# Optimization experiments

Hardware: AMD Instinct MI355X
Metric: run time of the kernel (lower is better)

## Reference

```python
import jax, jax.numpy as jnp
import numpy as np
import math

EMB = 512

def setup_inputs() -> dict:
    key = jax.random.key(0)
    ks = jax.random.split(key, 7)
    B, L, E = 4, 4096, EMB
    s = 1.0 / math.sqrt(E)
    return {
        "x": jax.random.normal(ks[0], (B, L, E), dtype=jnp.float32),
        "Wq": jax.random.normal(ks[1], (E, E), dtype=jnp.float32) * s,
        "bq": jax.random.normal(ks[2], (E,), dtype=jnp.float32) * 0.01,
        "Wk": jax.random.normal(ks[3], (E, E), dtype=jnp.float32) * s,
        "bk": jax.random.normal(ks[4], (E,), dtype=jnp.float32) * 0.01,
        "Wv": jax.random.normal(ks[5], (E, E), dtype=jnp.float32) * s,
        "bv": jax.random.normal(ks[6], (E,), dtype=jnp.float32) * 0.01,
    }

def reference(x, Wq, bq, Wk, bk, Wv, bv):
    # x: [B, L, E]; Linear weights stored torch-style [out, in]
    E = x.shape[-1]
    L = x.shape[1]
    q = jnp.einsum('ble,fe->blf', x, Wq) + bq
    k = jnp.einsum('ble,fe->blf', x, Wk) + bk
    v = jnp.einsum('ble,fe->blf', x, Wv) + bv
    qk = jnp.einsum('bqe,bke->bqk', q, k)  # [B, L, L]
    # causal mask: strict upper triangle filled with -1e9 BEFORE scaling (as in source)
    mask = jnp.triu(jnp.ones((L, L), dtype=bool), k=1)
    qk = jnp.where(mask, jnp.float32(-1e9), qk)
    att = jax.nn.softmax(qk / jnp.sqrt(jnp.float32(E)), axis=-1)
    return jnp.einsum('bqk,bke->bqe', att, v)
```

## Files before the change

### kernel.cpp

```cpp
#include <hip/hip_runtime.h>

typedef unsigned short u16;
typedef short bf16x8 __attribute__((ext_vector_type(8)));
typedef float f32x4 __attribute__((ext_vector_type(4)));
typedef u16 u16x8 __attribute__((ext_vector_type(8)));
typedef u16 u16x4 __attribute__((ext_vector_type(4)));

#define LQ   4096
#define EMB  512
#define NB   4
#define MROWS (NB * LQ)
#define QSCALE 0.04419417382415922f

__device__ __forceinline__ u16 f2bf(float f) {
  unsigned u = __builtin_bit_cast(unsigned, f);
  u += 0x7fffu + ((u >> 16) & 1u);
  return (u16)(u >> 16);
}
__device__ __forceinline__ float bf2f(u16 h) {
  unsigned u = ((unsigned)h) << 16;
  return __builtin_bit_cast(float, u);
}

__global__ void prep_w(const float* __restrict__ Wq, const float* __restrict__ bq,
                       const float* __restrict__ Wk, const float* __restrict__ bk,
                       const float* __restrict__ Wv, const float* __restrict__ bv,
                       u16* __restrict__ wqb, u16* __restrict__ wkb, u16* __restrict__ wvb,
                       float* __restrict__ bias) {
  int i = blockIdx.x * 256 + threadIdx.x;
  if (i < EMB * EMB) {
    wqb[i] = f2bf(Wq[i] * QSCALE);
    wkb[i] = f2bf(Wk[i]);
    wvb[i] = f2bf(Wv[i]);
  }
  if (i < EMB) {
    bias[i]           = bq[i] * QSCALE;
    bias[EMB + i]     = bk[i];
    bias[2 * EMB + i] = bv[i];
  }
}

__global__ void prep_x(const float* __restrict__ x, u16* __restrict__ xb) {
  int i = blockIdx.x * 256 + threadIdx.x;
  const float4* p = (const float4*)(x + (size_t)i * 8);
  float4 a = p[0], b = p[1];
  u16x8 o;
  o[0] = f2bf(a.x); o[1] = f2bf(a.y); o[2] = f2bf(a.z); o[3] = f2bf(a.w);
  o[4] = f2bf(b.x); o[5] = f2bf(b.y); o[6] = f2bf(b.z); o[7] = f2bf(b.w);
  *(u16x8*)(xb + (size_t)i * 8) = o;
}

__device__ __forceinline__ void gemm_tile_core(
    const u16* __restrict__ A, int lda,
    const u16* __restrict__ B, int ldb,
    int kIters, u16* ldsA, u16* ldsB,
    f32x4 acc[4][4], int tid, int lane, int wr, int wc)
{
  for (int kb = 0; kb < kIters; ++kb) {
    const u16* ga = A + kb * 64;
    const u16* gb = B + kb * 64;
#pragma unroll
    for (int p = 0; p < 4; ++p) {
      int c = tid + p * 256;
      int row = c >> 3, h = c & 7;
      int hh = h ^ (row & 7);
      uint4 va = *(const uint4*)(ga + (size_t)row * lda + h * 8);
      uint4 vb = *(const uint4*)(gb + (size_t)row * ldb + h * 8);
      *(uint4*)(ldsA + row * 64 + hh * 8) = va;
      *(uint4*)(ldsB + row * 64 + hh * 8) = vb;
    }
    __syncthreads();
#pragma unroll
    for (int s = 0; s < 2; ++s) {
      bf16x8 af[4], bf[4];
#pragma unroll
      for (int m = 0; m < 4; ++m) {
        int row = wr * 64 + m * 16 + (lane & 15);
        int hh = (s * 4 + (lane >> 4)) ^ (row & 7);
        af[m] = *(const bf16x8*)(ldsA + row * 64 + hh * 8);
      }
#pragma unroll
      for (int n = 0; n < 4; ++n) {
        int row = wc * 64 + n * 16 + (lane & 15);
        int hh = (s * 4 + (lane >> 4)) ^ (row & 7);
        bf[n] = *(const bf16x8*)(ldsB + row * 64 + hh * 8);
      }
#pragma unroll
      for (int m = 0; m < 4; ++m)
#pragma unroll
        for (int n = 0; n < 4; ++n)
          acc[m][n] = __builtin_amdgcn_mfma_f32_16x16x32_bf16(af[m], bf[n], acc[m][n], 0, 0, 0);
    }
    __syncthreads();
  }
}

template <int VT>
__global__ __launch_bounds__(256, 2) void k_qkv(
    const u16* __restrict__ xb, const u16* __restrict__ W,
    const float* __restrict__ bias, u16* __restrict__ out)
{
  __shared__ uint4 ldsraw[2048];
  u16* ldsA = (u16*)ldsraw;
  u16* ldsB = (u16*)(ldsraw + 1024);
  int bi = blockIdx.x;
  int rt = bi >> 2, ct = bi & 3;
  int tid = threadIdx.x, lane = tid & 63, wave = tid >> 6;
  int wr = wave >> 1, wc = wave & 1;
  f32x4 acc[4][4];
#pragma unroll
  for (int m = 0; m < 4; ++m)
#pragma unroll
    for (int n = 0; n < 4; ++n) acc[m][n] = (f32x4)0.0f;

  gemm_tile_core(xb + (size_t)rt * 128 * EMB, EMB,
                 W + (size_t)ct * 128 * EMB, EMB, EMB / 64,
                 ldsA, ldsB, acc, tid, lane, wr, wc);

#pragma unroll
  for (int m = 0; m < 4; ++m)
#pragma unroll
    for (int n = 0; n < 4; ++n) {
      int row0 = rt * 128 + wr * 64 + m * 16 + ((lane >> 4) << 2);
      int col  = ct * 128 + wc * 64 + n * 16 + (lane & 15);
      float bv = bias[col];
      if (VT == 0) {
#pragma unroll
        for (int r = 0; r < 4; ++r)
          out[(size_t)(row0 + r) * EMB + col] = f2bf(acc[m][n][r] + bv);
      } else {
        int b = row0 >> 12, l0 = row0 & (LQ - 1);
        u16x4 pk;
#pragma unroll
        for (int r = 0; r < 4; ++r) pk[r] = f2bf(acc[m][n][r] + bv);
        *(u16x4*)(out + ((size_t)(b * EMB + col)) * LQ + l0) = pk;
      }
    }
}

__global__ __launch_bounds__(256, 2) void k_qk(
    const u16* __restrict__ Q, const u16* __restrict__ K,
    u16* __restrict__ S, int bstart)
{
  __shared__ uint4 ldsraw[2048];
  u16* ldsA = (u16*)ldsraw;
  u16* ldsB = (u16*)(ldsraw + 1024);
  int t = blockIdx.x;
  int b_local = t / 528;
  int i = t - b_local * 528;
  int qi = (int)((sqrtf(8.f * (float)i + 1.f) - 1.f) * 0.5f);
  while ((qi + 1) * (qi + 2) / 2 <= i) ++qi;
  while (qi * (qi + 1) / 2 > i) --qi;
  int ki = i - qi * (qi + 1) / 2;
  int bg = bstart + b_local;

  int tid = threadIdx.x, lane = tid & 63, wave = tid >> 6;
  int wr = wave >> 1, wc = wave & 1;
  f32x4 acc[4][4];
#pragma unroll
  for (int m = 0; m < 4; ++m)
#pragma unroll
    for (int n = 0; n < 4; ++n) acc[m][n] = (f32x4)0.0f;

  gemm_tile_core(Q + ((size_t)bg * LQ + qi * 128) * EMB, EMB,
                 K + ((size_t)bg * LQ + ki * 128) * EMB, EMB, EMB / 64,
                 ldsA, ldsB, acc, tid, lane, wr, wc);

  u16* Sb = S + (size_t)b_local * LQ * LQ;
#pragma unroll
  for (int m = 0; m < 4; ++m)
#pragma unroll
    for (int n = 0; n < 4; ++n) {
      int row0 = qi * 128 + wr * 64 + m * 16 + ((lane >> 4) << 2);
      int col  = ki * 128 + wc * 64 + n * 16 + (lane & 15);
#pragma unroll
      for (int r = 0; r < 4; ++r) {
        int row = row0 + r;
        float v = (col > row) ? -1e9f : acc[m][n][r];
        Sb[(size_t)row * LQ + col] = f2bf(v);
      }
    }
}

__global__ __launch_bounds__(256) void k_softmax(u16* __restrict__ S)
{
  int rowb = blockIdx.x;
  int q = rowb & (LQ - 1);
  u16* sr = S + (size_t)rowb * LQ;
  int n = ((q >> 7) + 1) << 7;
  int tid = threadIdx.x;
  int lane = tid & 63, wave = tid >> 6;
  __shared__ float red[8];

  float v[16];
  float mx = -3.0e38f;
#pragma unroll
  for (int p = 0; p < 2; ++p) {
    int idx = (p * 256 + tid) * 8;
    if (idx < n) {
      u16x8 raw = *(const u16x8*)(sr + idx);
#pragma unroll
      for (int j = 0; j < 8; ++j) {
        float f = bf2f(raw[j]);
        v[p * 8 + j] = f;
        mx = fmaxf(mx, f);
      }
    }
  }
#pragma unroll
  for (int off = 32; off >= 1; off >>= 1) mx = fmaxf(mx, __shfl_xor(mx, off));
  if (lane == 0) red[wave] = mx;
  __syncthreads();
  if (tid == 0) red[4] = fmaxf(fmaxf(red[0], red[1]), fmaxf(red[2], red[3]));
  __syncthreads();
  mx = red[4];
  __syncthreads();

  float sum = 0.f;
#pragma unroll
  for (int p = 0; p < 2; ++p) {
    int idx = (p * 256 + tid) * 8;
    if (idx < n) {
#pragma unroll
      for (int j = 0; j < 8; ++j) {
        float e = __expf(v[p * 8 + j] - mx);
        v[p * 8 + j] = e;
        sum += e;
      }
    }
  }
#pragma unroll
  for (int off = 32; off >= 1; off >>= 1) sum += __shfl_xor(sum, off);
  if (lane == 0) red[wave] = sum;
  __syncthreads();
  if (tid == 0) red[4] = red[0] + red[1] + red[2] + red[3];
  __syncthreads();
  float inv = 1.0f / red[4];

#pragma unroll
  for (int p = 0; p < 2; ++p) {
    int idx = (p * 256 + tid) * 8;
    if (idx < n) {
      u16x8 o;
#pragma unroll
      for (int j = 0; j < 8; ++j) o[j] = f2bf(v[p * 8 + j] * inv);
      *(u16x8*)(sr + idx) = o;
    }
  }
}

__global__ __launch_bounds__(256, 2) void k_pv(
    const u16* __restrict__ P, const u16* __restrict__ Vt,
    float* __restrict__ out, int bstart, int bcount)
{
  __shared__ uint4 ldsraw[2048];
  u16* ldsA = (u16*)ldsraw;
  u16* ldsB = (u16*)(ldsraw + 1024);
  int bi = blockIdx.x;
  int per_rt = bcount * 4;
  int rt = 31 - bi / per_rt;
  int rem = bi % per_rt;
  int b_local = rem >> 2, ct = rem & 3;
  int bg = bstart + b_local;

  int tid = threadIdx.x, lane = tid & 63, wave = tid >> 6;
  int wr = wave >> 1, wc = wave & 1;
  f32x4 acc[4][4];
#pragma unroll
  for (int m = 0; m < 4; ++m)
#pragma unroll
    for (int n = 0; n < 4; ++n) acc[m][n] = (f32x4)0.0f;

  int kIters = (rt + 1) * 2;
  gemm_tile_core(P + (size_t)b_local * LQ * LQ + (size_t)rt * 128 * LQ, LQ,
                 Vt + ((size_t)bg * EMB + ct * 128) * LQ, LQ, kIters,
                 ldsA, ldsB, acc, tid, lane, wr, wc);

#pragma unroll
  for (int m = 0; m < 4; ++m)
#pragma unroll
    for (int n = 0; n < 4; ++n) {
      int row0 = rt * 128 + wr * 64 + m * 16 + ((lane >> 4) << 2);
      int col  = ct * 128 + wc * 64 + n * 16 + (lane & 15);
#pragma unroll
      for (int r = 0; r < 4; ++r)
        out[((size_t)bg * LQ + row0 + r) * EMB + col] = acc[m][n][r];
    }
}

extern "C" void kernel_launch(void* const* d_in, const int* in_sizes, int n_in,
                              void* d_out, int out_size, void* d_ws, size_t ws_size,
                              hipStream_t stream) {
  const float* x  = (const float*)d_in[0];
  const float* Wq = (const float*)d_in[1];
  const float* bq = (const float*)d_in[2];
  const float* Wk = (const float*)d_in[3];
  const float* bk = (const float*)d_in[4];
  const float* Wv = (const float*)d_in[5];
  const float* bv = (const float*)d_in[6];

  char* ws = (char*)d_ws;
  size_t off = 0;
  u16* xb  = (u16*)(ws + off); off += (size_t)MROWS * EMB * 2;
  u16* wqb = (u16*)(ws + off); off += (size_t)EMB * EMB * 2;
  u16* wkb = (u16*)(ws + off); off += (size_t)EMB * EMB * 2;
  u16* wvb = (u16*)(ws + off); off += (size_t)EMB * EMB * 2;
  float* bias = (float*)(ws + off); off += 3 * EMB * 4;
  off = (off + 255) & ~(size_t)255;
  u16* Qb  = (u16*)(ws + off); off += (size_t)MROWS * EMB * 2;
  u16* Kb  = (u16*)(ws + off); off += (size_t)MROWS * EMB * 2;
  u16* Vtb = (u16*)(ws + off); off += (size_t)MROWS * EMB * 2;
  size_t fixed = off;
  size_t s_full = (size_t)NB * LQ * LQ * 2;
  int bcap = (ws_size >= fixed + s_full) ? NB : 1;
  u16* Sb = (u16*)(ws + fixed);

  prep_w<<<(EMB * EMB + 255) / 256, 256, 0, stream>>>(Wq, bq, Wk, bk, Wv, bv,
                                                      wqb, wkb, wvb, bias);
  prep_x<<<(MROWS * EMB / 8) / 256, 256, 0, stream>>>(x, xb);

  k_qkv<0><<<512, 256, 0, stream>>>(xb, wqb, bias, Qb);
  k_qkv<0><<<512, 256, 0, stream>>>(xb, wkb, bias + EMB, Kb);
  k_qkv<1><<<512, 256, 0, stream>>>(xb, wvb, bias + 2 * EMB, Vtb);

  for (int bs = 0; bs < NB; bs += bcap) {
    int bc = (bs + bcap <= NB) ? bcap : (NB - bs);
    k_qk<<<528 * bc, 256, 0, stream>>>(Qb, Kb, Sb, bs);
    k_softmax<<<bc * LQ, 256, 0, stream>>>(Sb);
    k_pv<<<32 * bc * 4, 256, 0, stream>>>(Sb, Vtb, (float*)d_out, bs, bc);
  }
}
```

Before: 219.0 us.

## Use direct global-to-LDS loads, merge QKV launches, reorder PV tiles

Global-to-shared staging in the GEMM core now uses global_load_lds, which writes straight into LDS and skips the register round trip. The XOR swizzle moves from the LDS address to the global source address so the stored layout stays the same. The three QKV projection launches become one 1536-block launch, cutting launch count and keeping more blocks in flight. PV row tiles are also reordered so the long causal tiles go first and the short ones fill in after.

```diff
diff --git a/kernel.cpp b/kernel.cpp
--- a/kernel.cpp
+++ b/kernel.cpp
@@ -1,10 +1,14 @@
 #include <hip/hip_runtime.h>
 
 typedef unsigned short u16;
+typedef unsigned int u32;
 typedef short bf16x8 __attribute__((ext_vector_type(8)));
 typedef float f32x4 __attribute__((ext_vector_type(4)));
 typedef u16 u16x8 __attribute__((ext_vector_type(8)));
 typedef u16 u16x4 __attribute__((ext_vector_type(4)));
+
+typedef const __attribute__((address_space(1))) u32* gas_ptr;
+typedef __attribute__((address_space(3))) u32* las_ptr;
 
 #define LQ   4096
 #define EMB  512
@@ -56,23 +60,26 @@
     int kIters, u16* ldsA, u16* ldsB,
     f32x4 acc[4][4], int tid, int lane, int wr, int wc)
 {
+  int wave = tid >> 6;
   for (int kb = 0; kb < kIters; ++kb) {
     const u16* ga = A + kb * 64;
     const u16* gb = B + kb * 64;
 #pragma unroll
     for (int p = 0; p < 4; ++p) {
       int c = tid + p * 256;
-      int row = c >> 3, h = c & 7;
-      int hh = h ^ (row & 7);
-      uint4 va = *(const uint4*)(ga + (size_t)row * lda + h * 8);
-      uint4 vb = *(const uint4*)(gb + (size_t)row * ldb + h * 8);
-      *(uint4*)(ldsA + row * 64 + hh * 8) = va;
-      *(uint4*)(ldsB + row * 64 + hh * 8) = vb;
+      int row = c >> 3, hh = c & 7;
+      int h = hh ^ (row & 7);
+      const u16* sa = ga + (size_t)row * lda + h * 8;
+      const u16* sb = gb + (size_t)row * ldb + h * 8;
+      u16* la = ldsA + wave * 512 + p * 2048;
+      u16* lb = ldsB + wave * 512 + p * 2048;
+      __builtin_amdgcn_global_load_lds((gas_ptr)(const void*)sa, (las_ptr)(void*)la, 16, 0, 0);
+      __builtin_amdgcn_global_load_lds((gas_ptr)(const void*)sb, (las_ptr)(void*)lb, 16, 0, 0);
     }
     __syncthreads();
 #pragma unroll
     for (int s = 0; s < 2; ++s) {
-      bf16x8 af[4], bf[4];
+      bf16x8 af[4], bfr[4];
 #pragma unroll
       for (int m = 0; m < 4; ++m) {
         int row = wr * 64 + m * 16 + (lane & 15);
@@ -83,28 +90,33 @@
       for (int n = 0; n < 4; ++n) {
         int row = wc * 64 + n * 16 + (lane & 15);
         int hh = (s * 4 + (lane >> 4)) ^ (row & 7);
-        bf[n] = *(const bf16x8*)(ldsB + row * 64 + hh * 8);
+        bfr[n] = *(const bf16x8*)(ldsB + row * 64 + hh * 8);
       }
 #pragma unroll
       for (int m = 0; m < 4; ++m)
 #pragma unroll
         for (int n = 0; n < 4; ++n)
-          acc[m][n] = __builtin_amdgcn_mfma_f32_16x16x32_bf16(af[m], bf[n], acc[m][n], 0, 0, 0);
+          acc[m][n] = __builtin_amdgcn_mfma_f32_16x16x32_bf16(af[m], bfr[n], acc[m][n], 0, 0, 0);
     }
     __syncthreads();
   }
 }
 
-template <int VT>
 __global__ __launch_bounds__(256, 2) void k_qkv(
-    const u16* __restrict__ xb, const u16* __restrict__ W,
-    const float* __restrict__ bias, u16* __restrict__ out)
+    const u16* __restrict__ xb,
+    const u16* __restrict__ w0, const u16* __restrict__ w1, const u16* __restrict__ w2,
+    const float* __restrict__ bias,
+    u16* __restrict__ o0, u16* __restrict__ o1, u16* __restrict__ o2)
 {
   __shared__ uint4 ldsraw[2048];
   u16* ldsA = (u16*)ldsraw;
   u16* ldsB = (u16*)(ldsraw + 1024);
   int bi = blockIdx.x;
-  int rt = bi >> 2, ct = bi & 3;
+  int which = bi >> 9;
+  int t = bi & 511;
+  int rt = t >> 2, ct = t & 3;
+  const u16* W = (which == 0) ? w0 : (which == 1) ? w1 : w2;
+  const float* bs = bias + which * EMB;
   int tid = threadIdx.x, lane = tid & 63, wave = tid >> 6;
   int wr = wave >> 1, wc = wave & 1;
   f32x4 acc[4][4];
@@ -123,8 +135,9 @@
     for (int n = 0; n < 4; ++n) {
       int row0 = rt * 128 + wr * 64 + m * 16 + ((lane >> 4) << 2);
       int col  = ct * 128 + wc * 64 + n * 16 + (lane & 15);
-      float bv = bias[col];
-      if (VT == 0) {
+      float bv = bs[col];
+      if (which < 2) {
+        u16* out = (which == 0) ? o0 : o1;
 #pragma unroll
         for (int r = 0; r < 4; ++r)
           out[(size_t)(row0 + r) * EMB + col] = f2bf(acc[m][n][r] + bv);
@@ -133,7 +146,7 @@
         u16x4 pk;
 #pragma unroll
         for (int r = 0; r < 4; ++r) pk[r] = f2bf(acc[m][n][r] + bv);
-        *(u16x4*)(out + ((size_t)(b * EMB + col)) * LQ + l0) = pk;
+        *(u16x4*)(o2 + ((size_t)(b * EMB + col)) * LQ + l0) = pk;
       }
     }
 }
@@ -258,8 +271,9 @@
   u16* ldsB = (u16*)(ldsraw + 1024);
   int bi = blockIdx.x;
   int per_rt = bcount * 4;
-  int rt = 31 - bi / per_rt;
+  int idx = bi / per_rt;
   int rem = bi % per_rt;
+  int rt = (idx < 16) ? (31 - idx) : (idx - 16);
   int b_local = rem >> 2, ct = rem & 3;
   int bg = bstart + b_local;
 
@@ -319,9 +333,7 @@
                                                       wqb, wkb, wvb, bias);
   prep_x<<<(MROWS * EMB / 8) / 256, 256, 0, stream>>>(x, xb);
 
-  k_qkv<0><<<512, 256, 0, stream>>>(xb, wqb, bias, Qb);
-  k_qkv<0><<<512, 256, 0, stream>>>(xb, wkb, bias + EMB, Kb);
-  k_qkv<1><<<512, 256, 0, stream>>>(xb, wvb, bias + 2 * EMB, Vtb);
+  k_qkv<<<1536, 256, 0, stream>>>(xb, wqb, wkb, wvb, bias, Qb, Kb, Vtb);
 
   for (int bs = 0; bs < NB; bs += bcap) {
     int bc = (bs + bcap <= NB) ? bcap : (NB - bs);
```

New measurement: 211.9 us. -3.2%, faster.
